# Kernel optimization log

Measured on AMD Instinct MI355X. Metric: run time of the kernel, lower is better.

Reference implementation:

```python
import jax, jax.numpy as jnp
import numpy as np
from functools import partial

DIM = 128      # LSTM hidden size
NODES = 81     # graph nodes
T = 12         # sequence length


def _lstm_layer(x, Wih, Whh, bih, bhh):
    """PyTorch-style LSTM layer. x: (N, T, in) -> (N, T, H). Gate order i,f,g,o."""
    N = x.shape[0]
    H = Whh.shape[1]
    b = bih + bhh

    def step(carry, xt):
        h, c = carry
        gates = xt @ Wih.T + h @ Whh.T + b              # (N, 4H)
        i, f, g, o = jnp.split(gates, 4, axis=-1)
        i = jax.nn.sigmoid(i)
        f = jax.nn.sigmoid(f)
        g = jnp.tanh(g)
        o = jax.nn.sigmoid(o)
        c = f * c + i * g
        h = o * jnp.tanh(c)
        return (h, c), h

    h0 = jnp.zeros((N, H), x.dtype)
    c0 = jnp.zeros((N, H), x.dtype)
    xT = jnp.swapaxes(x, 0, 1)                           # (T, N, in)
    _, hs = jax.lax.scan(step, (h0, c0), xT)
    return jnp.swapaxes(hs, 0, 1)                        # (N, T, H)


def setup_inputs() -> dict:
    key = jax.random.key(0)
    ks = jax.random.split(key, 16)
    k = 1.0 / np.sqrt(DIM)
    u = lambda kk, shape: jax.random.uniform(kk, shape, jnp.float32, -k, k)
    inp = {
        "g_data": jax.random.normal(ks[0], (512, T, NODES), jnp.float32),
        "weights": jax.random.normal(ks[1], (NODES, NODES), jnp.float32) * 0.1,
        # LSTM layer 0 (input size 1)
        "Wih0": u(ks[2], (4 * DIM, 1)),
        "Whh0": u(ks[3], (4 * DIM, DIM)),
        "bih0": u(ks[4], (4 * DIM,)),
        "bhh0": u(ks[5], (4 * DIM,)),
        # LSTM layer 1 (input size DIM)
        "Wih1": u(ks[6], (4 * DIM, DIM)),
        "Whh1": u(ks[7], (4 * DIM, DIM)),
        "bih1": u(ks[8], (4 * DIM,)),
        "bhh1": u(ks[9], (4 * DIM,)),
        # MLP head 128 -> 32 -> 1
        "fc1_w": u(ks[10], (32, DIM)),
        "fc1_b": u(ks[11], (32,)),
        "fc2_w": u(ks[12], (1, 32)),
        "fc2_b": u(ks[13], (1,)),
    }
    return inp


def reference(g_data, weights, Wih0, Whh0, bih0, bhh0, Wih1, Whh1, bih1, bhh1,
              fc1_w, fc1_b, fc2_w, fc2_b):
    B = g_data.shape[0]
    # Vectorized graph aggregation: income[:, :, i] = g_data @ weights[:, i]
    income = jnp.einsum('bta,an->bnt', g_data, weights)   # (B, 81, 12)
    x = income.reshape(B * NODES, T, 1)                   # one scalar seq per (sample, node)
    h1 = _lstm_layer(x, Wih0, Whh0, bih0, bhh0)           # (B*81, 12, 128)
    h2 = _lstm_layer(h1, Wih1, Whh1, bih1, bhh1)          # (B*81, 12, 128)
    last = h2[:, -1, :]                                   # only last step feeds the output
    hid = jax.nn.relu(last @ fc1_w.T + fc1_b)             # (B*81, 32)
    out = jax.nn.relu(hid @ fc2_w.T + fc2_b)              # (B*81, 1)
    return out.reshape(B, NODES).reshape(B, 1, NODES, 1)
```

## Files before the change

kernel.cpp:

```cpp
#include <hip/hip_runtime.h>
#include <math.h>

#define NODES 81
#define T_STEPS 12
#define NSEQ 41472
#define HID 128
#define SEQB 16

typedef unsigned short ushort;
typedef unsigned int uint;
typedef __attribute__((ext_vector_type(8))) _Float16 half8;
typedef __attribute__((ext_vector_type(4))) float f32x4;

#define MFMA(A, B, C) __builtin_amdgcn_mfma_f32_16x16x32_f16((A), (B), (C), 0, 0, 0)

__device__ __forceinline__ float sigf(float v) {
    return __builtin_amdgcn_rcpf(1.f + __builtin_amdgcn_exp2f(v * -1.442695041f));
}
__device__ __forceinline__ float tanhf_(float v) {
    return fmaf(2.f, __builtin_amdgcn_rcpf(1.f + __builtin_amdgcn_exp2f(v * -2.885390082f)), -1.f);
}

__global__ void prep_kernel(const float* __restrict__ Whh0,
                            const float* __restrict__ Wih1,
                            const float* __restrict__ Whh1,
                            const float* __restrict__ Wih0,
                            const float* __restrict__ bih0, const float* __restrict__ bhh0,
                            const float* __restrict__ bih1, const float* __restrict__ bhh1,
                            _Float16* __restrict__ WF0,
                            _Float16* __restrict__ WF1i,
                            _Float16* __restrict__ WF1h,
                            float* __restrict__ wq,
                            float* __restrict__ b0q,
                            float* __restrict__ b1q)
{
    int idx = blockIdx.x * 256 + threadIdx.x;
    if (idx < 196608) {
        int mat = idx >> 16;
        int li  = idx & 65535;
        int j   = li & 7;
        int l   = (li >> 3) & 63;
        int nt  = (li >> 9) & 31;
        int ks  = li >> 14;
        int k = ks * 32 + (l >> 4) * 8 + j;
        int n = nt * 16 + (l & 15);
        const float* W = (mat == 0) ? Whh0 : (mat == 1 ? Wih1 : Whh1);
        _Float16* D = (mat == 0) ? WF0 : (mat == 1 ? WF1i : WF1h);
        D[li] = (_Float16)W[n * 128 + k];
    } else if (idx < 197120) {
        int jp = idx - 196608;
        int u = jp >> 2, t4 = jp & 3;
        wq[jp] = Wih0[t4 * 128 + u];
    } else if (idx < 197632) {
        int jp = idx - 197120;
        int u = jp >> 2, t4 = jp & 3;
        b0q[jp] = bih0[t4 * 128 + u] + bhh0[t4 * 128 + u];
    } else if (idx < 198144) {
        int jp = idx - 197632;
        int u = jp >> 2, t4 = jp & 3;
        b1q[jp] = bih1[t4 * 128 + u] + bhh1[t4 * 128 + u];
    }
}

__global__ void income_kernel(const float* __restrict__ g_data,
                              const float* __restrict__ w,
                              float* __restrict__ x)
{
    int idx = blockIdx.x * 256 + threadIdx.x;
    int n = idx % NODES;
    int r = idx / NODES;
    int t = r % T_STEPS;
    int b = r / T_STEPS;
    const float* grow = g_data + (b * T_STEPS + t) * NODES;
    float s = 0.f;
    #pragma unroll 3
    for (int a = 0; a < NODES; ++a)
        s += grow[a] * w[a * NODES + n];
    x[t * NSEQ + b * NODES + n] = s;
}

__global__ __launch_bounds__(512, 1) void lstm_main(
    const float* __restrict__ x,
    const _Float16* __restrict__ WF0,
    const _Float16* __restrict__ WF1i,
    const _Float16* __restrict__ WF1h,
    const float* __restrict__ wq,
    const float* __restrict__ b0q,
    const float* __restrict__ b1q,
    const float* __restrict__ fc1_w,
    const float* __restrict__ fc1_b,
    const float* __restrict__ fc2_w,
    const float* __restrict__ fc2_b,
    float* __restrict__ out)
{
    __shared__ __align__(16) _Float16 hA0[4096];
    __shared__ __align__(16) _Float16 hA1[4096];

    const int tid = threadIdx.x;
    const int l   = tid & 63;
    const int gr  = tid >> 6;
    const int l15 = l & 15;
    const int l16 = l >> 4;
    const int u   = gr * 16 + l15;
    const int seq0 = blockIdx.x * SEQB;

    for (int i = tid; i < 2048; i += 512) {
        ((uint*)hA0)[i] = 0u; ((uint*)hA1)[i] = 0u;
    }

    const _Float16* wfb0 = WF0  + gr * 512 + l * 8;
    const _Float16* wfb1 = WF1i + gr * 512 + l * 8;
    const _Float16* wfb2 = WF1h + gr * 512 + l * 8;
    half8 B0[4][4], B1[4][4], B2[4][4];
    #pragma unroll
    for (int ks = 0; ks < 4; ++ks)
        #pragma unroll
        for (int t4 = 0; t4 < 4; ++t4) {
            B0[ks][t4] = *(const half8*)(wfb0 + ks * 16384 + t4 * 4096);
            B1[ks][t4] = *(const half8*)(wfb1 + ks * 16384 + t4 * 4096);
            B2[ks][t4] = *(const half8*)(wfb2 + ks * 16384 + t4 * 4096);
        }

    const float4 wv  = *(const float4*)(wq  + u * 4);
    const float4 bv0 = *(const float4*)(b0q + u * 4);
    const float4 bv1 = *(const float4*)(b1q + u * 4);

    float c0[4], c1[4];
    #pragma unroll
    for (int i = 0; i < 4; ++i) { c0[i] = 0.f; c1[i] = 0.f; }
    __syncthreads();

    const int wrbase = (u >> 3) * 128 + (u & 7);

    int cur = 0;
    for (int t = 0; t < T_STEPS; ++t) {
        const int nxt = cur ^ 1;
        const float4 xv4 = *(const float4*)(x + t * NSEQ + seq0 + l16 * 4);

        f32x4 acc[4];

        #pragma unroll
        for (int t4 = 0; t4 < 4; ++t4) acc[t4] = (f32x4){0.f, 0.f, 0.f, 0.f};
        #pragma unroll
        for (int ks = 0; ks < 4; ++ks) {
            half8 a = *(const half8*)(hA0 + cur * 2048 + (ks * 4 + l16) * 128 + l15 * 8);
            #pragma unroll
            for (int t4 = 0; t4 < 4; ++t4) acc[t4] = MFMA(a, B0[ks][t4], acc[t4]);
        }
        #pragma unroll
        for (int r = 0; r < 4; ++r) {
            int m = l16 * 4 + r;
            float gi = acc[0][r] + xv4[r] * wv.x + bv0.x;
            float gf = acc[1][r] + xv4[r] * wv.y + bv0.y;
            float gg = acc[2][r] + xv4[r] * wv.z + bv0.z;
            float go = acc[3][r] + xv4[r] * wv.w + bv0.w;
            float iv = sigf(gi), fv = sigf(gf), gv = tanhf_(gg), ov = sigf(go);
            float c = fv * c0[r] + iv * gv;
            c0[r] = c;
            hA0[nxt * 2048 + wrbase + m * 8] = (_Float16)(ov * tanhf_(c));
        }
        __syncthreads();

        #pragma unroll
        for (int t4 = 0; t4 < 4; ++t4) acc[t4] = (f32x4){0.f, 0.f, 0.f, 0.f};
        #pragma unroll
        for (int ks = 0; ks < 4; ++ks) {
            half8 a = *(const half8*)(hA0 + nxt * 2048 + (ks * 4 + l16) * 128 + l15 * 8);
            #pragma unroll
            for (int t4 = 0; t4 < 4; ++t4) acc[t4] = MFMA(a, B1[ks][t4], acc[t4]);
        }
        #pragma unroll
        for (int ks = 0; ks < 4; ++ks) {
            half8 a = *(const half8*)(hA1 + cur * 2048 + (ks * 4 + l16) * 128 + l15 * 8);
            #pragma unroll
            for (int t4 = 0; t4 < 4; ++t4) acc[t4] = MFMA(a, B2[ks][t4], acc[t4]);
        }
        #pragma unroll
        for (int r = 0; r < 4; ++r) {
            int m = l16 * 4 + r;
            float gi = acc[0][r] + bv1.x;
            float gf = acc[1][r] + bv1.y;
            float gg = acc[2][r] + bv1.z;
            float go = acc[3][r] + bv1.w;
            float iv = sigf(gi), fv = sigf(gf), gv = tanhf_(gg), ov = sigf(go);
            float c = fv * c1[r] + iv * gv;
            c1[r] = c;
            hA1[nxt * 2048 + wrbase + m * 8] = (_Float16)(ov * tanhf_(c));
        }
        cur = nxt;
    }
    __syncthreads();

    float* hidb = (float*)hA0;
    {
        int s = tid >> 5, j = tid & 31;
        float sum = fc1_b[j];
        const float* wrow = fc1_w + j * HID;
        #pragma unroll 4
        for (int kq = 0; kq < 16; ++kq) {
            half8 H = *(const half8*)(hA1 + cur * 2048 + kq * 128 + s * 8);
            #pragma unroll
            for (int j8 = 0; j8 < 8; ++j8)
                sum += (float)H[j8] * wrow[kq * 8 + j8];
        }
        float hv = fmaxf(sum, 0.f);
        __syncthreads();
        hidb[s * 33 + j] = hv;
    }
    __syncthreads();
    if (tid < SEQB) {
        float sum = fc2_b[0];
        #pragma unroll
        for (int j = 0; j < 32; ++j) sum += hidb[tid * 33 + j] * fc2_w[j];
        out[seq0 + tid] = fmaxf(sum, 0.f);
    }
}

extern "C" void kernel_launch(void* const* d_in, const int* in_sizes, int n_in,
                              void* d_out, int out_size, void* d_ws, size_t ws_size,
                              hipStream_t stream)
{
    const float* g_data = (const float*)d_in[0];
    const float* weights = (const float*)d_in[1];
    const float* Wih0   = (const float*)d_in[2];
    const float* Whh0   = (const float*)d_in[3];
    const float* bih0   = (const float*)d_in[4];
    const float* bhh0   = (const float*)d_in[5];
    const float* Wih1   = (const float*)d_in[6];
    const float* Whh1   = (const float*)d_in[7];
    const float* bih1   = (const float*)d_in[8];
    const float* bhh1   = (const float*)d_in[9];
    const float* fc1_w  = (const float*)d_in[10];
    const float* fc1_b  = (const float*)d_in[11];
    const float* fc2_w  = (const float*)d_in[12];
    const float* fc2_b  = (const float*)d_in[13];
    float* out = (float*)d_out;

    float* ws = (float*)d_ws;
    float*     x    = ws;
    _Float16*  WF0  = (_Float16*)(x + NSEQ * T_STEPS);
    _Float16*  WF1i = WF0 + 65536;
    _Float16*  WF1h = WF1i + 65536;
    float*     wqp  = (float*)(WF1h + 65536);
    float*     b0q  = wqp + 512;
    float*     b1q  = b0q + 512;

    prep_kernel<<<774, 256, 0, stream>>>(Whh0, Wih1, Whh1, Wih0, bih0, bhh0, bih1, bhh1,
                                         WF0, WF1i, WF1h, wqp, b0q, b1q);
    income_kernel<<<1944, 256, 0, stream>>>(g_data, weights, x);
    lstm_main<<<NSEQ / SEQB, 512, 0, stream>>>(x, WF0, WF1i, WF1h, wqp, b0q, b1q,
                                               fc1_w, fc1_b, fc2_w, fc2_b, out);
}
```

Baseline: 383.6 us.

## Double sequences per block and stage layer-0 recurrent weights in LDS

The LSTM block now handles 32 sequences with 1024 threads, and two wave groups split the M dimension. The layer-0 recurrent weight fragments are copied once into shared memory and read from it inside the timestep loop, instead of being held in registers. The aim is to share weight loads across more sequences and to lower per-thread register pressure so larger blocks fit. In exchange, every step adds LDS read traffic for the B operands, uses about 160KB of LDS per block, and the layer-1 weights still need 128 VGPRs per thread under a 1024-thread launch bound, so register spilling is possible.

```diff
diff --git a/kernel.cpp b/kernel.cpp
--- a/kernel.cpp
+++ b/kernel.cpp
@@ -5,7 +5,7 @@
 #define T_STEPS 12
 #define NSEQ 41472
 #define HID 128
-#define SEQB 16
+#define SEQB 32
 
 typedef unsigned short ushort;
 typedef unsigned int uint;
@@ -79,7 +79,7 @@
     x[t * NSEQ + b * NODES + n] = s;
 }
 
-__global__ __launch_bounds__(512, 1) void lstm_main(
+__global__ __launch_bounds__(1024, 1) void lstm_main(
     const float* __restrict__ x,
     const _Float16* __restrict__ WF0,
     const _Float16* __restrict__ WF1i,
@@ -93,30 +93,33 @@
     const float* __restrict__ fc2_b,
     float* __restrict__ out)
 {
-    __shared__ __align__(16) _Float16 hA0[4096];
-    __shared__ __align__(16) _Float16 hA1[4096];
+    __shared__ __align__(16) _Float16 WF0s[65536];
+    __shared__ __align__(16) _Float16 hA0[8192];
+    __shared__ __align__(16) _Float16 hA1[8192];
 
     const int tid = threadIdx.x;
     const int l   = tid & 63;
-    const int gr  = tid >> 6;
+    const int w   = tid >> 6;
+    const int gr  = w & 7;
+    const int mt  = w >> 3;
     const int l15 = l & 15;
     const int l16 = l >> 4;
     const int u   = gr * 16 + l15;
     const int seq0 = blockIdx.x * SEQB;
 
-    for (int i = tid; i < 2048; i += 512) {
+    for (int i = tid; i < 8192; i += 1024)
+        ((float4*)WF0s)[i] = ((const float4*)WF0)[i];
+    for (int i = tid; i < 4096; i += 1024) {
         ((uint*)hA0)[i] = 0u; ((uint*)hA1)[i] = 0u;
     }
 
-    const _Float16* wfb0 = WF0  + gr * 512 + l * 8;
     const _Float16* wfb1 = WF1i + gr * 512 + l * 8;
     const _Float16* wfb2 = WF1h + gr * 512 + l * 8;
-    half8 B0[4][4], B1[4][4], B2[4][4];
+    half8 B1[4][4], B2[4][4];
     #pragma unroll
     for (int ks = 0; ks < 4; ++ks)
         #pragma unroll
         for (int t4 = 0; t4 < 4; ++t4) {
-            B0[ks][t4] = *(const half8*)(wfb0 + ks * 16384 + t4 * 4096);
             B1[ks][t4] = *(const half8*)(wfb1 + ks * 16384 + t4 * 4096);
             B2[ks][t4] = *(const half8*)(wfb2 + ks * 16384 + t4 * 4096);
         }
@@ -130,12 +133,13 @@
     for (int i = 0; i < 4; ++i) { c0[i] = 0.f; c1[i] = 0.f; }
     __syncthreads();
 
-    const int wrbase = (u >> 3) * 128 + (u & 7);
+    const int wrbase = (u >> 3) * 256 + (u & 7);
+    const _Float16* wfb0s = WF0s + gr * 512 + l * 8;
 
     int cur = 0;
     for (int t = 0; t < T_STEPS; ++t) {
         const int nxt = cur ^ 1;
-        const float4 xv4 = *(const float4*)(x + t * NSEQ + seq0 + l16 * 4);
+        const float4 xv4 = *(const float4*)(x + t * NSEQ + seq0 + mt * 16 + l16 * 4);
 
         f32x4 acc[4];
 
@@ -143,13 +147,16 @@
         for (int t4 = 0; t4 < 4; ++t4) acc[t4] = (f32x4){0.f, 0.f, 0.f, 0.f};
         #pragma unroll
         for (int ks = 0; ks < 4; ++ks) {
-            half8 a = *(const half8*)(hA0 + cur * 2048 + (ks * 4 + l16) * 128 + l15 * 8);
-            #pragma unroll
-            for (int t4 = 0; t4 < 4; ++t4) acc[t4] = MFMA(a, B0[ks][t4], acc[t4]);
+            half8 a = *(const half8*)(hA0 + cur * 4096 + (ks * 4 + l16) * 256 + l15 * 8 + mt * 128);
+            #pragma unroll
+            for (int t4 = 0; t4 < 4; ++t4) {
+                half8 b = *(const half8*)(wfb0s + ks * 16384 + t4 * 4096);
+                acc[t4] = MFMA(a, b, acc[t4]);
+            }
         }
         #pragma unroll
         for (int r = 0; r < 4; ++r) {
-            int m = l16 * 4 + r;
+            int m = mt * 16 + l16 * 4 + r;
             float gi = acc[0][r] + xv4[r] * wv.x + bv0.x;
             float gf = acc[1][r] + xv4[r] * wv.y + bv0.y;
             float gg = acc[2][r] + xv4[r] * wv.z + bv0.z;
@@ -157,7 +164,7 @@
             float iv = sigf(gi), fv = sigf(gf), gv = tanhf_(gg), ov = sigf(go);
             float c = fv * c0[r] + iv * gv;
             c0[r] = c;
-            hA0[nxt * 2048 + wrbase + m * 8] = (_Float16)(ov * tanhf_(c));
+            hA0[nxt * 4096 + wrbase + m * 8] = (_Float16)(ov * tanhf_(c));
         }
         __syncthreads();
 
@@ -165,19 +172,19 @@
         for (int t4 = 0; t4 < 4; ++t4) acc[t4] = (f32x4){0.f, 0.f, 0.f, 0.f};
         #pragma unroll
         for (int ks = 0; ks < 4; ++ks) {
-            half8 a = *(const half8*)(hA0 + nxt * 2048 + (ks * 4 + l16) * 128 + l15 * 8);
+            half8 a = *(const half8*)(hA0 + nxt * 4096 + (ks * 4 + l16) * 256 + l15 * 8 + mt * 128);
             #pragma unroll
             for (int t4 = 0; t4 < 4; ++t4) acc[t4] = MFMA(a, B1[ks][t4], acc[t4]);
         }
         #pragma unroll
         for (int ks = 0; ks < 4; ++ks) {
-            half8 a = *(const half8*)(hA1 + cur * 2048 + (ks * 4 + l16) * 128 + l15 * 8);
+            half8 a = *(const half8*)(hA1 + cur * 4096 + (ks * 4 + l16) * 256 + l15 * 8 + mt * 128);
             #pragma unroll
             for (int t4 = 0; t4 < 4; ++t4) acc[t4] = MFMA(a, B2[ks][t4], acc[t4]);
         }
         #pragma unroll
         for (int r = 0; r < 4; ++r) {
-            int m = l16 * 4 + r;
+            int m = mt * 16 + l16 * 4 + r;
             float gi = acc[0][r] + bv1.x;
             float gf = acc[1][r] + bv1.y;
             float gg = acc[2][r] + bv1.z;
@@ -185,20 +192,20 @@
             float iv = sigf(gi), fv = sigf(gf), gv = tanhf_(gg), ov = sigf(go);
             float c = fv * c1[r] + iv * gv;
             c1[r] = c;
-            hA1[nxt * 2048 + wrbase + m * 8] = (_Float16)(ov * tanhf_(c));
+            hA1[nxt * 4096 + wrbase + m * 8] = (_Float16)(ov * tanhf_(c));
         }
         cur = nxt;
     }
     __syncthreads();
 
-    float* hidb = (float*)hA0;
+    float* hidb = (float*)WF0s;
     {
         int s = tid >> 5, j = tid & 31;
         float sum = fc1_b[j];
         const float* wrow = fc1_w + j * HID;
         #pragma unroll 4
         for (int kq = 0; kq < 16; ++kq) {
-            half8 H = *(const half8*)(hA1 + cur * 2048 + kq * 128 + s * 8);
+            half8 H = *(const half8*)(hA1 + cur * 4096 + kq * 256 + s * 8);
             #pragma unroll
             for (int j8 = 0; j8 < 8; ++j8)
                 sum += (float)H[j8] * wrow[kq * 8 + j8];
@@ -248,6 +255,6 @@
     prep_kernel<<<774, 256, 0, stream>>>(Whh0, Wih1, Whh1, Wih0, bih0, bhh0, bih1, bhh1,
                                          WF0, WF1i, WF1h, wqp, b0q, b1q);
     income_kernel<<<1944, 256, 0, stream>>>(g_data, weights, x);
-    lstm_main<<<NSEQ / SEQB, 512, 0, stream>>>(x, WF0, WF1i, WF1h, wqp, b0q, b1q,
-                                               fc1_w, fc1_b, fc2_w, fc2_b, out);
-}
+    lstm_main<<<NSEQ / SEQB, 1024, 0, stream>>>(x, WF0, WF1i, WF1h, wqp, b0q, b1q,
+                                                fc1_w, fc1_b, fc2_w, fc2_b, out);
+}
```

After: 909.0 us. 2.37x slower.
